# Optimization experiments

Measured on AMD Instinct MI355X. Metric: run time of the kernel, lower is better.

The kernel has to match this reference:

```python
import jax, jax.numpy as jnp
import numpy as np

N_NODES = 400000
NUM_GRAPHS = 2048
IN_FEAT = 256
DENSE = 128
N_HEADS = 8


def setup_inputs() -> dict:
    key = jax.random.key(0)
    k_h, k_seg, k_w1, k_b1, k_w2, k_b2 = jax.random.split(key, 6)
    h = jax.random.normal(k_h, (N_NODES, IN_FEAT), dtype=jnp.float32)
    segment_ids = jnp.sort(
        jax.random.randint(k_seg, (N_NODES,), 0, NUM_GRAPHS, dtype=jnp.int32))
    # Linear params (jax convention: x @ W + b)
    W1 = jax.random.normal(k_w1, (IN_FEAT, DENSE), dtype=jnp.float32) / np.sqrt(IN_FEAT)
    b1 = jax.random.normal(k_b1, (DENSE,), dtype=jnp.float32) * 0.01
    W2 = jax.random.normal(k_w2, (DENSE, N_HEADS), dtype=jnp.float32) / np.sqrt(DENSE)
    b2 = jax.random.normal(k_b2, (N_HEADS,), dtype=jnp.float32) * 0.01
    return {"h": h, "segment_ids": segment_ids, "W1": W1, "b1": b1,
            "W2": W2, "b2": b2, "num_graphs": NUM_GRAPHS}


def reference(h, segment_ids, W1, b1, W2, b2, num_graphs):
    # scores: fc2(tanh(fc1(h))) -> [N, n_heads]
    scores = jnp.tanh(h @ W1 + b1) @ W2 + b2
    # ragged (per-graph) softmax over nodes, per head (dgl.softmax_nodes)
    seg_max = jax.ops.segment_max(scores, segment_ids, num_segments=num_graphs)  # [G, H]
    ex = jnp.exp(scores - seg_max[segment_ids])                                  # [N, H]
    denom = jax.ops.segment_sum(ex, segment_ids, num_segments=num_graphs)        # [G, H]
    attn = ex / denom[segment_ids]                                               # [N, H]
    # mean over heads of per-head weighted segment sums == segment sum with
    # head-averaged weights (linearity), avoiding H separate ndata passes.
    w = attn.mean(axis=1)                                                         # [N]
    out = jax.ops.segment_sum(h * w[:, None], segment_ids, num_segments=num_graphs)  # [G, in_feat]
    return out
```

## Files before the change

### kernel.cpp

```cpp
#include <hip/hip_runtime.h>
#include <hip/hip_bf16.h>

#define IN_FEAT 256
#define DENSE   128
#define NHEADS  8
#define MAXN    328
#define TILE    32
#define LDA     264
#define LDT2    136

typedef __attribute__((ext_vector_type(8))) short bf16x8_t;
typedef __attribute__((ext_vector_type(4))) float f32x4_t;

__device__ __forceinline__ unsigned int f2bf(float f) {
  unsigned int u = __float_as_uint(f);
  u += 0x7fffu + ((u >> 16) & 1u);
  return u >> 16;
}

__device__ __forceinline__ unsigned int f2bf_hu(float f) {
  return (__float_as_uint(f) + 0x8000u) >> 16;
}

__device__ __forceinline__ float bf2f(short s) {
  return __uint_as_float(((unsigned int)(unsigned short)s) << 16);
}

__device__ __forceinline__ float fast_tanh(float x) {
  float ax = fabsf(x);
  float e = __expf(-2.0f * ax);
  float t = (1.0f - e) / (1.0f + e);
  return copysignf(t, x);
}

__global__ void w1_frag_kernel(const float* __restrict__ W1, unsigned int* __restrict__ w1f) {
  int t = blockIdx.x * blockDim.x + threadIdx.x;
  if (t >= 4096) return;
  int lane = t & 63;
  int fid  = t >> 6;
  int ct = fid & 1;
  int ks = (fid >> 1) & 7;
  int wv = fid >> 4;
  int col = wv * 32 + ct * 16 + (lane & 15);
  int k0  = ks * 32 + (lane >> 4) * 8;
  unsigned int p[4];
  #pragma unroll
  for (int jj = 0; jj < 4; ++jj) {
    unsigned int lo = f2bf(W1[(size_t)(k0 + 2 * jj) * DENSE + col]);
    unsigned int hi = f2bf(W1[(size_t)(k0 + 2 * jj + 1) * DENSE + col]);
    p[jj] = lo | (hi << 16);
  }
  *(uint4*)&w1f[(size_t)t * 4] = make_uint4(p[0], p[1], p[2], p[3]);
}

__global__ void w2_frag_kernel(const float* __restrict__ W2, unsigned int* __restrict__ w2f) {
  int t = threadIdx.x;
  if (t >= 256) return;
  int lane = t & 63, ks = t >> 6;
  int hd = lane & 15, q = lane >> 4;
  unsigned int p[4];
  #pragma unroll
  for (int jj = 0; jj < 4; ++jj) {
    int k0 = ks * 32 + q * 8 + 2 * jj;
    unsigned int lo = (hd < 8) ? f2bf(W2[k0 * NHEADS + hd]) : 0u;
    unsigned int hi = (hd < 8) ? f2bf(W2[(k0 + 1) * NHEADS + hd]) : 0u;
    p[jj] = lo | (hi << 16);
  }
  *(uint4*)&w2f[(size_t)t * 4] = make_uint4(p[0], p[1], p[2], p[3]);
}

__device__ __forceinline__ int lower_bound_dev(const int* __restrict__ seg, int N, int v) {
  int lo = 0, hi = N;
  while (lo < hi) {
    int mid = (lo + hi) >> 1;
    if (seg[mid] < v) lo = mid + 1; else hi = mid;
  }
  return lo;
}

__launch_bounds__(256, 3)
__global__ void scorepool_kernel(const float* __restrict__ h,
                                 const int* __restrict__ seg,
                                 const unsigned int* __restrict__ w1f,
                                 const unsigned int* __restrict__ w2f,
                                 const float* __restrict__ b1,
                                 const float* __restrict__ b2,
                                 float* __restrict__ S,
                                 float* __restrict__ D,
                                 int N) {
  __shared__ short sA[TILE * LDA];
  __shared__ short sTb[TILE * LDT2];
  __shared__ float sEx[TILE * NHEADS];
  __shared__ int   sSeg[TILE];
  __shared__ float sB1[DENSE];
  __shared__ float sB2[NHEADS];

  const int tid  = threadIdx.x;
  const int row0 = blockIdx.x * TILE;
  const int rem  = N - row0;
  const int mcnt = rem < TILE ? rem : TILE;

  const int lane = tid & 63;
  const int wv   = tid >> 6;
  const int lr   = lane & 15;
  const int q    = lane >> 4;
  const int q8   = q * 8;
  const int pfr  = tid >> 6;
  const int pfc4 = (tid & 63) * 4;

  if (tid < DENSE)  sB1[tid] = b1[tid];
  if (tid < NHEADS) sB2[tid] = b2[tid];
  if (tid < TILE) {
    int r = row0 + tid;
    int rlast = row0 + mcnt - 1;
    sSeg[tid] = seg[r <= rlast ? r : rlast];
  }

  #pragma unroll
  for (int it = 0; it < 8; ++it) {
    int row = it * 4 + pfr;
    float4 v = make_float4(0.f, 0.f, 0.f, 0.f);
    if (row < mcnt) v = *(const float4*)(h + (size_t)(row0 + row) * IN_FEAT + pfc4);
    unsigned int p0 = f2bf_hu(v.x) | (f2bf_hu(v.y) << 16);
    unsigned int p1 = f2bf_hu(v.z) | (f2bf_hu(v.w) << 16);
    *(uint2*)&sA[row * LDA + pfc4] = make_uint2(p0, p1);
  }
  __syncthreads();

  {
    f32x4_t a00 = {0,0,0,0}, a01 = {0,0,0,0}, a10 = {0,0,0,0}, a11 = {0,0,0,0};
    const bf16x8_t* w1fv = (const bf16x8_t*)w1f;
    #pragma unroll
    for (int ks = 0; ks < 8; ++ks) {
      bf16x8_t av0 = *(const bf16x8_t*)&sA[(     lr) * LDA + ks * 32 + q8];
      bf16x8_t av1 = *(const bf16x8_t*)&sA[(16 + lr) * LDA + ks * 32 + q8];
      int f0 = ((wv * 8 + ks) * 2) * 64 + lane;
      bf16x8_t wf0 = w1fv[f0];
      bf16x8_t wf1 = w1fv[f0 + 64];
      a00 = __builtin_amdgcn_mfma_f32_16x16x32_bf16(av0, wf0, a00, 0, 0, 0);
      a01 = __builtin_amdgcn_mfma_f32_16x16x32_bf16(av0, wf1, a01, 0, 0, 0);
      a10 = __builtin_amdgcn_mfma_f32_16x16x32_bf16(av1, wf0, a10, 0, 0, 0);
      a11 = __builtin_amdgcn_mfma_f32_16x16x32_bf16(av1, wf1, a11, 0, 0, 0);
    }
    float bias0 = sB1[wv * 32 + lr];
    float bias1 = sB1[wv * 32 + 16 + lr];
    #pragma unroll
    for (int r = 0; r < 4; ++r) {
      a00[r] = fast_tanh(a00[r] + bias0);
      a01[r] = fast_tanh(a01[r] + bias1);
      a10[r] = fast_tanh(a10[r] + bias0);
      a11[r] = fast_tanh(a11[r] + bias1);
    }
    #pragma unroll
    for (int r = 0; r < 4; ++r) {
      int row0r = q * 4 + r, row1r = 16 + q * 4 + r;
      sTb[row0r * LDT2 + wv * 32 + lr]      = (short)f2bf(a00[r]);
      sTb[row0r * LDT2 + wv * 32 + 16 + lr] = (short)f2bf(a01[r]);
      sTb[row1r * LDT2 + wv * 32 + lr]      = (short)f2bf(a10[r]);
      sTb[row1r * LDT2 + wv * 32 + 16 + lr] = (short)f2bf(a11[r]);
    }
  }
  __syncthreads();

  if (wv < 2) {
    const bf16x8_t* w2fv = (const bf16x8_t*)w2f;
    float bias = (lr < 8) ? sB2[lr] : 0.0f;
    f32x4_t c = {bias, bias, bias, bias};
    #pragma unroll
    for (int ks = 0; ks < 4; ++ks) {
      bf16x8_t at = *(const bf16x8_t*)&sTb[(wv * 16 + lr) * LDT2 + ks * 32 + q8];
      bf16x8_t wf = w2fv[ks * 64 + lane];
      c = __builtin_amdgcn_mfma_f32_16x16x32_bf16(at, wf, c, 0, 0, 0);
    }
    #pragma unroll
    for (int r = 0; r < 4; ++r) {
      int ridx = wv * 16 + q * 4 + r;
      if (lr < 8) sEx[ridx * NHEADS + lr] = (ridx < mcnt) ? __expf(c[r]) : 0.0f;
    }
  }
  __syncthreads();

  {
    const int c = tid;
    float acc[NHEADS];
    #pragma unroll
    for (int hh = 0; hh < NHEADS; ++hh) acc[hh] = 0.f;
    int curg = sSeg[0];
    for (int i = 0; i < TILE; ++i) {
      int gi = sSeg[i];
      if (gi != curg) {
        #pragma unroll
        for (int hh = 0; hh < NHEADS; ++hh) {
          unsafeAtomicAdd(&S[((size_t)curg * NHEADS + hh) * IN_FEAT + c], acc[hh]);
          acc[hh] = 0.f;
        }
        curg = gi;
      }
      float hv = bf2f(sA[i * LDA + c]);
      float4 e0 = *(const float4*)&sEx[i * NHEADS];
      float4 e1 = *(const float4*)&sEx[i * NHEADS + 4];
      acc[0] = fmaf(e0.x, hv, acc[0]); acc[1] = fmaf(e0.y, hv, acc[1]);
      acc[2] = fmaf(e0.z, hv, acc[2]); acc[3] = fmaf(e0.w, hv, acc[3]);
      acc[4] = fmaf(e1.x, hv, acc[4]); acc[5] = fmaf(e1.y, hv, acc[5]);
      acc[6] = fmaf(e1.z, hv, acc[6]); acc[7] = fmaf(e1.w, hv, acc[7]);
    }
    #pragma unroll
    for (int hh = 0; hh < NHEADS; ++hh)
      unsafeAtomicAdd(&S[((size_t)curg * NHEADS + hh) * IN_FEAT + c], acc[hh]);
  }

  if (tid < NHEADS) {
    const int hh = tid;
    float d = 0.f;
    int curg = sSeg[0];
    for (int i = 0; i < TILE; ++i) {
      int gi = sSeg[i];
      if (gi != curg) {
        unsafeAtomicAdd(&D[(size_t)curg * NHEADS + hh], d);
        d = 0.f; curg = gi;
      }
      d += sEx[i * NHEADS + hh];
    }
    unsafeAtomicAdd(&D[(size_t)curg * NHEADS + hh], d);
  }
}

__global__ void finalize_kernel(const float* __restrict__ S,
                                const float* __restrict__ D,
                                float* __restrict__ out) {
  __shared__ float sInv[NHEADS];
  const int g = blockIdx.x, c = threadIdx.x;
  if (c < NHEADS) {
    float d = D[(size_t)g * NHEADS + c];
    sInv[c] = (d > 0.f) ? (1.0f / d) : 0.f;
  }
  __syncthreads();
  float s = 0.f;
  #pragma unroll
  for (int hh = 0; hh < NHEADS; ++hh)
    s = fmaf(S[((size_t)g * NHEADS + hh) * IN_FEAT + c], sInv[hh], s);
  out[(size_t)g * IN_FEAT + c] = 0.125f * s;
}

__launch_bounds__(256, 3)
__global__ void attn_pool_fused(const float* __restrict__ h,
                                const int* __restrict__ seg,
                                const float* __restrict__ W1,
                                const float* __restrict__ b1,
                                const float* __restrict__ W2,
                                const float* __restrict__ b2,
                                float* __restrict__ out,
                                int N) {
  __shared__ short sA[64 * LDA];
  __shared__ float sScores[MAXN * NHEADS];
  __shared__ float sWgt[MAXN];
  __shared__ float sW2T[NHEADS * 132];
  __shared__ float sB1[DENSE];
  __shared__ float sB2[NHEADS];
  __shared__ float sRed[256];
  __shared__ float sMax[NHEADS];
  __shared__ float sInvD[NHEADS];

  const int g   = blockIdx.x;
  const int tid = threadIdx.x;

  int start = lower_bound_dev(seg, N, g);
  int end   = lower_bound_dev(seg, N, g + 1);
  int n = end - start;
  if (n > MAXN) n = MAXN;
  float* sT = (float*)sA;

  if (n == 0) {
    if (tid < IN_FEAT) out[(size_t)g * IN_FEAT + tid] = 0.0f;
    return;
  }

  for (int idx = tid; idx < DENSE * NHEADS; idx += 256) {
    int k = idx >> 3; int hd = idx & 7;
    sW2T[hd * 132 + k] = W2[idx];
  }
  if (tid < DENSE)  sB1[tid] = b1[tid];
  if (tid < NHEADS) sB2[tid] = b2[tid];

  const int lane = tid & 63;
  const int wv   = tid >> 6;
  const int lr   = lane & 15;
  const int q    = lane >> 4;
  bf16x8_t b1f[16];
  #pragma unroll
  for (int ct = 0; ct < 2; ++ct) {
    int colb = wv * 32 + ct * 16 + lr;
    #pragma unroll
    for (int ks = 0; ks < 8; ++ks) {
      bf16x8_t bb;
      #pragma unroll
      for (int j = 0; j < 8; ++j)
        bb[j] = (short)f2bf(W1[(ks * 32 + q * 8 + j) * DENSE + colb]);
      b1f[ct * 8 + ks] = bb;
    }
  }

  const int ntiles = (n + 63) >> 6;
  for (int t = 0; t < ntiles; ++t) {
    const int m0   = start + t * 64;
    const int rem  = n - t * 64;
    const int mcnt = rem < 64 ? rem : 64;
    __syncthreads();
    #pragma unroll
    for (int it = 0; it < 16; ++it) {
      int row = it * 4 + (tid >> 6);
      int f4  = tid & 63;
      float4 v = make_float4(0.f, 0.f, 0.f, 0.f);
      if (row < mcnt) v = *(const float4*)(h + (size_t)(m0 + row) * IN_FEAT + f4 * 4);
      unsigned int p0 = f2bf(v.x) | (f2bf(v.y) << 16);
      unsigned int p1 = f2bf(v.z) | (f2bf(v.w) << 16);
      *(uint2*)&sA[row * LDA + f4 * 4] = make_uint2(p0, p1);
    }
    __syncthreads();
    f32x4_t acc[4][2];
    #pragma unroll
    for (int mt = 0; mt < 4; ++mt) {
      acc[mt][0] = (f32x4_t){0, 0, 0, 0};
      acc[mt][1] = (f32x4_t){0, 0, 0, 0};
    }
    #pragma unroll
    for (int ks = 0; ks < 8; ++ks) {
      bf16x8_t a0 = *(const bf16x8_t*)&sA[( 0 + lr) * LDA + ks * 32 + q * 8];
      bf16x8_t a1 = *(const bf16x8_t*)&sA[(16 + lr) * LDA + ks * 32 + q * 8];
      bf16x8_t a2 = *(const bf16x8_t*)&sA[(32 + lr) * LDA + ks * 32 + q * 8];
      bf16x8_t a3 = *(const bf16x8_t*)&sA[(48 + lr) * LDA + ks * 32 + q * 8];
      acc[0][0] = __builtin_amdgcn_mfma_f32_16x16x32_bf16(a0, b1f[ks],     acc[0][0], 0, 0, 0);
      acc[0][1] = __builtin_amdgcn_mfma_f32_16x16x32_bf16(a0, b1f[8 + ks], acc[0][1], 0, 0, 0);
      acc[1][0] = __builtin_amdgcn_mfma_f32_16x16x32_bf16(a1, b1f[ks],     acc[1][0], 0, 0, 0);
      acc[1][1] = __builtin_amdgcn_mfma_f32_16x16x32_bf16(a1, b1f[8 + ks], acc[1][1], 0, 0, 0);
      acc[2][0] = __builtin_amdgcn_mfma_f32_16x16x32_bf16(a2, b1f[ks],     acc[2][0], 0, 0, 0);
      acc[2][1] = __builtin_amdgcn_mfma_f32_16x16x32_bf16(a2, b1f[8 + ks], acc[2][1], 0, 0, 0);
      acc[3][0] = __builtin_amdgcn_mfma_f32_16x16x32_bf16(a3, b1f[ks],     acc[3][0], 0, 0, 0);
      acc[3][1] = __builtin_amdgcn_mfma_f32_16x16x32_bf16(a3, b1f[8 + ks], acc[3][1], 0, 0, 0);
    }
    __syncthreads();
    #pragma unroll
    for (int mt = 0; mt < 4; ++mt) {
      int rbase = mt * 16 + q * 4;
      #pragma unroll
      for (int ct = 0; ct < 2; ++ct) {
        int col = wv * 32 + ct * 16 + lr;
        float bias = sB1[col];
        #pragma unroll
        for (int r = 0; r < 4; ++r)
          sT[(rbase + r) * 132 + col] = fast_tanh(acc[mt][ct][r] + bias);
      }
    }
    __syncthreads();
    {
      int i0 = tid >> 3;
      int hd = tid & 7;
      #pragma unroll
      for (int half = 0; half < 2; ++half) {
        int i = i0 + half * 32;
        if (i < mcnt) {
          float s = sB2[hd];
          #pragma unroll
          for (int k4 = 0; k4 < DENSE; k4 += 4) {
            float4 tv  = *(const float4*)&sT[i * 132 + k4];
            float4 wv2 = *(const float4*)&sW2T[hd * 132 + k4];
            s = fmaf(tv.x, wv2.x, s); s = fmaf(tv.y, wv2.y, s);
            s = fmaf(tv.z, wv2.z, s); s = fmaf(tv.w, wv2.w, s);
          }
          sScores[(t * 64 + i) * NHEADS + hd] = s;
        }
      }
    }
  }
  __syncthreads();

  {
    const int hd = tid & 7, ch = tid >> 3;
    float m = -3.4e38f;
    for (int i = ch; i < n; i += 32) m = fmaxf(m, sScores[i * NHEADS + hd]);
    sRed[tid] = m;
    __syncthreads();
    if (tid < NHEADS) {
      float mm = sRed[tid];
      #pragma unroll
      for (int j = 1; j < 32; ++j) mm = fmaxf(mm, sRed[j * 8 + tid]);
      sMax[tid] = mm;
    }
    __syncthreads();
    float mm = sMax[hd], ssum = 0.f;
    for (int i = ch; i < n; i += 32) {
      float e = __expf(sScores[i * NHEADS + hd] - mm);
      sScores[i * NHEADS + hd] = e;
      ssum += e;
    }
    sRed[tid] = ssum;
    __syncthreads();
    if (tid < NHEADS) {
      float d = 0.f;
      #pragma unroll
      for (int j = 0; j < 32; ++j) d += sRed[j * 8 + tid];
      sInvD[tid] = 1.0f / d;
    }
    __syncthreads();
    for (int i = tid; i < n; i += 256) {
      float w = 0.f;
      #pragma unroll
      for (int hd2 = 0; hd2 < NHEADS; ++hd2) w += sScores[i * NHEADS + hd2] * sInvD[hd2];
      sWgt[i] = 0.125f * w;
    }
    __syncthreads();
  }

  {
    int grp = tid >> 6;
    int c4  = lane << 2;
    float4 acc = make_float4(0.f, 0.f, 0.f, 0.f);
    for (int i = grp; i < n; i += 4) {
      float w = sWgt[i];
      float4 hv = *(const float4*)(h + (size_t)(start + i) * IN_FEAT + c4);
      acc.x = fmaf(w, hv.x, acc.x);
      acc.y = fmaf(w, hv.y, acc.y);
      acc.z = fmaf(w, hv.z, acc.z);
      acc.w = fmaf(w, hv.w, acc.w);
    }
    float* sPart = (float*)sA;
    *(float4*)&sPart[grp * IN_FEAT + c4] = acc;
    __syncthreads();
    {
      float o = 0.f;
      #pragma unroll
      for (int p = 0; p < 4; ++p) o += sPart[p * IN_FEAT + tid];
      out[(size_t)g * IN_FEAT + tid] = o;
    }
  }
}

extern "C" void kernel_launch(void* const* d_in, const int* in_sizes, int n_in,
                              void* d_out, int out_size, void* d_ws, size_t ws_size,
                              hipStream_t stream) {
  const float* h   = (const float*)d_in[0];
  const int*   seg = (const int*)d_in[1];
  const float* W1  = (const float*)d_in[2];
  const float* b1v = (const float*)d_in[3];
  const float* W2  = (const float*)d_in[4];
  const float* b2v = (const float*)d_in[5];
  float* out = (float*)d_out;
  const int N = in_sizes[0] / IN_FEAT;
  const int G = out_size / IN_FEAT;

  const size_t w1f_bytes = 4096 * 16;
  const size_t w2f_bytes = 256 * 16;
  const size_t S_off   = (w1f_bytes + w2f_bytes + 255) & ~(size_t)255;
  const size_t S_bytes = (size_t)G * NHEADS * IN_FEAT * sizeof(float);
  const size_t D_off   = S_off + S_bytes;
  const size_t D_bytes = (size_t)G * NHEADS * sizeof(float);

  if (ws_size >= D_off + D_bytes) {
    unsigned int* w1f = (unsigned int*)d_ws;
    unsigned int* w2f = (unsigned int*)((char*)d_ws + w1f_bytes);
    float* S  = (float*)((char*)d_ws + S_off);
    float* Dp = (float*)((char*)d_ws + D_off);
    hipMemsetAsync((char*)d_ws + S_off, 0, S_bytes + D_bytes, stream);
    w1_frag_kernel<<<16, 256, 0, stream>>>(W1, w1f);
    w2_frag_kernel<<<1, 256, 0, stream>>>(W2, w2f);
    scorepool_kernel<<<(N + TILE - 1) / TILE, 256, 0, stream>>>(
        h, seg, w1f, w2f, b1v, b2v, S, Dp, N);
    finalize_kernel<<<G, 256, 0, stream>>>(S, Dp, out);
  } else {
    attn_pool_fused<<<G, 256, 0, stream>>>(h, seg, W1, b1v, W2, b2v, out, N);
  }
}
```

Measured before the change: 223.0 us.

## Process multiple row sub-tiles per block and carry segment accumulators across them

Each block now loops over several 32-row sub-tiles and keeps its per-segment S and D partial sums in registers across sub-tiles. Atomic flushes to global memory happen only when the segment id changes or at the end of the block. The goal is to cut the large number of per-tile global atomics, since segments span many rows. In exchange the grid shrinks considerably and each block runs the load/compute stages serially without prefetching, which reduces latency hiding from parallel blocks.

Result: slower. 233.9 us (+4.9%).

```diff
diff --git a/kernel.cpp b/kernel.cpp
--- a/kernel.cpp
+++ b/kernel.cpp
@@ -6,6 +6,7 @@
 #define NHEADS  8
 #define MAXN    328
 #define TILE    32
+#define NSUB    8
 #define LDA     264
 #define LDT2    136
 
@@ -96,9 +97,7 @@
   __shared__ float sB2[NHEADS];
 
   const int tid  = threadIdx.x;
-  const int row0 = blockIdx.x * TILE;
-  const int rem  = N - row0;
-  const int mcnt = rem < TILE ? rem : TILE;
+  const int blk0 = blockIdx.x * (TILE * NSUB);
 
   const int lane = tid & 63;
   const int wv   = tid >> 6;
@@ -110,119 +109,123 @@
 
   if (tid < DENSE)  sB1[tid] = b1[tid];
   if (tid < NHEADS) sB2[tid] = b2[tid];
-  if (tid < TILE) {
-    int r = row0 + tid;
-    int rlast = row0 + mcnt - 1;
-    sSeg[tid] = seg[r <= rlast ? r : rlast];
-  }
-
-  #pragma unroll
-  for (int it = 0; it < 8; ++it) {
-    int row = it * 4 + pfr;
-    float4 v = make_float4(0.f, 0.f, 0.f, 0.f);
-    if (row < mcnt) v = *(const float4*)(h + (size_t)(row0 + row) * IN_FEAT + pfc4);
-    unsigned int p0 = f2bf_hu(v.x) | (f2bf_hu(v.y) << 16);
-    unsigned int p1 = f2bf_hu(v.z) | (f2bf_hu(v.w) << 16);
-    *(uint2*)&sA[row * LDA + pfc4] = make_uint2(p0, p1);
-  }
-  __syncthreads();
-
-  {
-    f32x4_t a00 = {0,0,0,0}, a01 = {0,0,0,0}, a10 = {0,0,0,0}, a11 = {0,0,0,0};
-    const bf16x8_t* w1fv = (const bf16x8_t*)w1f;
-    #pragma unroll
-    for (int ks = 0; ks < 8; ++ks) {
-      bf16x8_t av0 = *(const bf16x8_t*)&sA[(     lr) * LDA + ks * 32 + q8];
-      bf16x8_t av1 = *(const bf16x8_t*)&sA[(16 + lr) * LDA + ks * 32 + q8];
-      int f0 = ((wv * 8 + ks) * 2) * 64 + lane;
-      bf16x8_t wf0 = w1fv[f0];
-      bf16x8_t wf1 = w1fv[f0 + 64];
-      a00 = __builtin_amdgcn_mfma_f32_16x16x32_bf16(av0, wf0, a00, 0, 0, 0);
-      a01 = __builtin_amdgcn_mfma_f32_16x16x32_bf16(av0, wf1, a01, 0, 0, 0);
-      a10 = __builtin_amdgcn_mfma_f32_16x16x32_bf16(av1, wf0, a10, 0, 0, 0);
-      a11 = __builtin_amdgcn_mfma_f32_16x16x32_bf16(av1, wf1, a11, 0, 0, 0);
-    }
-    float bias0 = sB1[wv * 32 + lr];
-    float bias1 = sB1[wv * 32 + 16 + lr];
-    #pragma unroll
-    for (int r = 0; r < 4; ++r) {
-      a00[r] = fast_tanh(a00[r] + bias0);
-      a01[r] = fast_tanh(a01[r] + bias1);
-      a10[r] = fast_tanh(a10[r] + bias0);
-      a11[r] = fast_tanh(a11[r] + bias1);
-    }
-    #pragma unroll
-    for (int r = 0; r < 4; ++r) {
-      int row0r = q * 4 + r, row1r = 16 + q * 4 + r;
-      sTb[row0r * LDT2 + wv * 32 + lr]      = (short)f2bf(a00[r]);
-      sTb[row0r * LDT2 + wv * 32 + 16 + lr] = (short)f2bf(a01[r]);
-      sTb[row1r * LDT2 + wv * 32 + lr]      = (short)f2bf(a10[r]);
-      sTb[row1r * LDT2 + wv * 32 + 16 + lr] = (short)f2bf(a11[r]);
-    }
-  }
-  __syncthreads();
-
-  if (wv < 2) {
-    const bf16x8_t* w2fv = (const bf16x8_t*)w2f;
-    float bias = (lr < 8) ? sB2[lr] : 0.0f;
-    f32x4_t c = {bias, bias, bias, bias};
-    #pragma unroll
-    for (int ks = 0; ks < 4; ++ks) {
-      bf16x8_t at = *(const bf16x8_t*)&sTb[(wv * 16 + lr) * LDT2 + ks * 32 + q8];
-      bf16x8_t wf = w2fv[ks * 64 + lane];
-      c = __builtin_amdgcn_mfma_f32_16x16x32_bf16(at, wf, c, 0, 0, 0);
-    }
-    #pragma unroll
-    for (int r = 0; r < 4; ++r) {
-      int ridx = wv * 16 + q * 4 + r;
-      if (lr < 8) sEx[ridx * NHEADS + lr] = (ridx < mcnt) ? __expf(c[r]) : 0.0f;
-    }
-  }
-  __syncthreads();
-
-  {
-    const int c = tid;
-    float acc[NHEADS];
-    #pragma unroll
-    for (int hh = 0; hh < NHEADS; ++hh) acc[hh] = 0.f;
-    int curg = sSeg[0];
+
+  float s0 = 0.f, s1 = 0.f, s2 = 0.f, s3 = 0.f;
+  float s4 = 0.f, s5 = 0.f, s6 = 0.f, s7 = 0.f;
+  float accD = 0.f;
+  int curg = seg[blk0];
+  const int c    = tid;
+  const int hsel = tid & 7;
+
+#define FLUSH_SD() {                                                                   \
+    float* Sp_ = &S[(size_t)curg * (NHEADS * IN_FEAT) + c];                            \
+    unsafeAtomicAdd(Sp_ + 0 * IN_FEAT, s0); s0 = 0.f;                                  \
+    unsafeAtomicAdd(Sp_ + 1 * IN_FEAT, s1); s1 = 0.f;                                  \
+    unsafeAtomicAdd(Sp_ + 2 * IN_FEAT, s2); s2 = 0.f;                                  \
+    unsafeAtomicAdd(Sp_ + 3 * IN_FEAT, s3); s3 = 0.f;                                  \
+    unsafeAtomicAdd(Sp_ + 4 * IN_FEAT, s4); s4 = 0.f;                                  \
+    unsafeAtomicAdd(Sp_ + 5 * IN_FEAT, s5); s5 = 0.f;                                  \
+    unsafeAtomicAdd(Sp_ + 6 * IN_FEAT, s6); s6 = 0.f;                                  \
+    unsafeAtomicAdd(Sp_ + 7 * IN_FEAT, s7); s7 = 0.f;                                  \
+    if (tid < NHEADS) unsafeAtomicAdd(&D[(size_t)curg * NHEADS + hsel], accD);         \
+    accD = 0.f;                                                                        \
+  }
+
+  for (int st = 0; st < NSUB; ++st) {
+    const int m0 = blk0 + st * TILE;
+    if (m0 >= N) break;
+    const int rem  = N - m0;
+    const int mcnt = rem < TILE ? rem : TILE;
+
+    __syncthreads();
+
+    if (tid < TILE) {
+      int r = m0 + tid;
+      sSeg[tid] = seg[r < N ? r : (N - 1)];
+    }
+    #pragma unroll
+    for (int it = 0; it < 8; ++it) {
+      int row = it * 4 + pfr;
+      float4 v = make_float4(0.f, 0.f, 0.f, 0.f);
+      if (row < mcnt) v = *(const float4*)(h + (size_t)(m0 + row) * IN_FEAT + pfc4);
+      unsigned int p0 = f2bf_hu(v.x) | (f2bf_hu(v.y) << 16);
+      unsigned int p1 = f2bf_hu(v.z) | (f2bf_hu(v.w) << 16);
+      *(uint2*)&sA[row * LDA + pfc4] = make_uint2(p0, p1);
+    }
+    __syncthreads();
+
+    {
+      f32x4_t a00 = {0,0,0,0}, a01 = {0,0,0,0}, a10 = {0,0,0,0}, a11 = {0,0,0,0};
+      const bf16x8_t* w1fv = (const bf16x8_t*)w1f;
+      #pragma unroll
+      for (int ks = 0; ks < 8; ++ks) {
+        bf16x8_t av0 = *(const bf16x8_t*)&sA[(     lr) * LDA + ks * 32 + q8];
+        bf16x8_t av1 = *(const bf16x8_t*)&sA[(16 + lr) * LDA + ks * 32 + q8];
+        int f0 = ((wv * 8 + ks) * 2) * 64 + lane;
+        bf16x8_t wf0 = w1fv[f0];
+        bf16x8_t wf1 = w1fv[f0 + 64];
+        a00 = __builtin_amdgcn_mfma_f32_16x16x32_bf16(av0, wf0, a00, 0, 0, 0);
+        a01 = __builtin_amdgcn_mfma_f32_16x16x32_bf16(av0, wf1, a01, 0, 0, 0);
+        a10 = __builtin_amdgcn_mfma_f32_16x16x32_bf16(av1, wf0, a10, 0, 0, 0);
+        a11 = __builtin_amdgcn_mfma_f32_16x16x32_bf16(av1, wf1, a11, 0, 0, 0);
+      }
+      float bias0 = sB1[wv * 32 + lr];
+      float bias1 = sB1[wv * 32 + 16 + lr];
+      #pragma unroll
+      for (int r = 0; r < 4; ++r) {
+        a00[r] = fast_tanh(a00[r] + bias0);
+        a01[r] = fast_tanh(a01[r] + bias1);
+        a10[r] = fast_tanh(a10[r] + bias0);
+        a11[r] = fast_tanh(a11[r] + bias1);
+      }
+      #pragma unroll
+      for (int r = 0; r < 4; ++r) {
+        int row0r = q * 4 + r, row1r = 16 + q * 4 + r;
+        sTb[row0r * LDT2 + wv * 32 + lr]      = (short)f2bf(a00[r]);
+        sTb[row0r * LDT2 + wv * 32 + 16 + lr] = (short)f2bf(a01[r]);
+        sTb[row1r * LDT2 + wv * 32 + lr]      = (short)f2bf(a10[r]);
+        sTb[row1r * LDT2 + wv * 32 + 16 + lr] = (short)f2bf(a11[r]);
+      }
+    }
+    __syncthreads();
+
+    if (wv < 2) {
+      const bf16x8_t* w2fv = (const bf16x8_t*)w2f;
+      float bias = (lr < 8) ? sB2[lr] : 0.0f;
+      f32x4_t cc = {bias, bias, bias, bias};
+      #pragma unroll
+      for (int ks = 0; ks < 4; ++ks) {
+        bf16x8_t at = *(const bf16x8_t*)&sTb[(wv * 16 + lr) * LDT2 + ks * 32 + q8];
+        bf16x8_t wf = w2fv[ks * 64 + lane];
+        cc = __builtin_amdgcn_mfma_f32_16x16x32_bf16(at, wf, cc, 0, 0, 0);
+      }
+      #pragma unroll
+      for (int r = 0; r < 4; ++r) {
+        int ridx = wv * 16 + q * 4 + r;
+        if (lr < 8) sEx[ridx * NHEADS + lr] = (ridx < mcnt) ? __expf(cc[r]) : 0.0f;
+      }
+    }
+    __syncthreads();
+
+    #pragma unroll 4
     for (int i = 0; i < TILE; ++i) {
       int gi = sSeg[i];
       if (gi != curg) {
-        #pragma unroll
-        for (int hh = 0; hh < NHEADS; ++hh) {
-          unsafeAtomicAdd(&S[((size_t)curg * NHEADS + hh) * IN_FEAT + c], acc[hh]);
-          acc[hh] = 0.f;
-        }
+        FLUSH_SD();
         curg = gi;
       }
-      float hv = bf2f(sA[i * LDA + c]);
+      float hv  = bf2f(sA[i * LDA + c]);
       float4 e0 = *(const float4*)&sEx[i * NHEADS];
       float4 e1 = *(const float4*)&sEx[i * NHEADS + 4];
-      acc[0] = fmaf(e0.x, hv, acc[0]); acc[1] = fmaf(e0.y, hv, acc[1]);
-      acc[2] = fmaf(e0.z, hv, acc[2]); acc[3] = fmaf(e0.w, hv, acc[3]);
-      acc[4] = fmaf(e1.x, hv, acc[4]); acc[5] = fmaf(e1.y, hv, acc[5]);
-      acc[6] = fmaf(e1.z, hv, acc[6]); acc[7] = fmaf(e1.w, hv, acc[7]);
-    }
-    #pragma unroll
-    for (int hh = 0; hh < NHEADS; ++hh)
-      unsafeAtomicAdd(&S[((size_t)curg * NHEADS + hh) * IN_FEAT + c], acc[hh]);
-  }
-
-  if (tid < NHEADS) {
-    const int hh = tid;
-    float d = 0.f;
-    int curg = sSeg[0];
-    for (int i = 0; i < TILE; ++i) {
-      int gi = sSeg[i];
-      if (gi != curg) {
-        unsafeAtomicAdd(&D[(size_t)curg * NHEADS + hh], d);
-        d = 0.f; curg = gi;
-      }
-      d += sEx[i * NHEADS + hh];
-    }
-    unsafeAtomicAdd(&D[(size_t)curg * NHEADS + hh], d);
-  }
+      s0 = fmaf(e0.x, hv, s0); s1 = fmaf(e0.y, hv, s1);
+      s2 = fmaf(e0.z, hv, s2); s3 = fmaf(e0.w, hv, s3);
+      s4 = fmaf(e1.x, hv, s4); s5 = fmaf(e1.y, hv, s5);
+      s6 = fmaf(e1.z, hv, s6); s7 = fmaf(e1.w, hv, s7);
+      accD += sEx[i * NHEADS + hsel];
+    }
+  }
+  FLUSH_SD();
+#undef FLUSH_SD
 }
 
 __global__ void finalize_kernel(const float* __restrict__ S,
@@ -463,7 +466,8 @@
     hipMemsetAsync((char*)d_ws + S_off, 0, S_bytes + D_bytes, stream);
     w1_frag_kernel<<<16, 256, 0, stream>>>(W1, w1f);
     w2_frag_kernel<<<1, 256, 0, stream>>>(W2, w2f);
-    scorepool_kernel<<<(N + TILE - 1) / TILE, 256, 0, stream>>>(
+    const int rows_per_block = TILE * NSUB;
+    scorepool_kernel<<<(N + rows_per_block - 1) / rows_per_block, 256, 0, stream>>>(
         h, seg, w1f, w2f, b1v, b2v, S, Dp, N);
     finalize_kernel<<<G, 256, 0, stream>>>(S, Dp, out);
   } else {
```
